# Kernel optimization log

Hardware: AMD Instinct MI355X
Metric: run time of the kernel (lower is better)

The kernel has to match this reference:

```python
import jax, jax.numpy as jnp
import numpy as np

BETA = 0.25
NUM_EMBEDDINGS = 2048
EMBEDDING_DIM = 512
N_TOKENS = 32768


def setup_inputs() -> dict:
    key = jax.random.key(0)
    k_z, k_e = jax.random.split(key)
    z = jax.random.normal(k_z, (N_TOKENS, EMBEDDING_DIM), dtype=jnp.float32)
    # nn.Embedding weight init: uniform(-1/K, 1/K)
    lim = 1.0 / NUM_EMBEDDINGS
    embedding = jax.random.uniform(
        k_e, (NUM_EMBEDDINGS, EMBEDDING_DIM), dtype=jnp.float32,
        minval=-lim, maxval=lim)
    return {"z": z, "embedding": embedding}


def reference(z, embedding):
    # z: [N, D], embedding: [K, D]
    z = z.reshape(-1, EMBEDDING_DIM)
    # squared euclidean distance: ||z||^2 + ||e||^2 - 2 z e^T  -> [N, K]
    d = (jnp.sum(z * z, axis=1, keepdims=True)
         + jnp.sum(embedding * embedding, axis=1)
         - 2.0 * jnp.matmul(z, embedding.T))
    min_encoding_indices = jnp.argmin(d, axis=1)[:, None]          # [N, 1]
    z_q = embedding[min_encoding_indices[:, 0]]                    # [N, D] gather

    sg = jax.lax.stop_gradient
    loss = jnp.mean((sg(z_q) - z) ** 2) + BETA * jnp.mean((z_q - sg(z)) ** 2)

    # straight-through estimator
    z_q_st = z + sg(z_q - z)

    # avg_probs = mean of one-hot encodings == normalized code-usage histogram
    n = z.shape[0]
    counts = jnp.zeros((NUM_EMBEDDINGS,), dtype=z.dtype).at[
        min_encoding_indices[:, 0]].add(1.0)
    avg_probs = counts / n
    perplexity = jnp.exp(-jnp.sum(avg_probs * jnp.log(avg_probs + 1e-10)))

    return (z_q_st, min_encoding_indices, loss, perplexity)
```

## Files before the change

kernel.cpp:

```cpp
#include <hip/hip_runtime.h>
#include <hip/hip_bf16.h>

#define N_TOK 32768
#define DIM   512
#define NE    2048

#define IDX_OFF  (N_TOK * DIM)
#define LOSS_OFF (IDX_OFF + N_TOK)
#define PERP_OFF (LOSS_OFF + 1)

#define KB(x) ((size_t)(x) << 10)
#define EPS 4e-4f

typedef __attribute__((ext_vector_type(8))) short bf16x8;
typedef __attribute__((ext_vector_type(4))) float f32x4;

__device__ inline unsigned short f2bf(float f) {
  unsigned int x = __float_as_uint(f);
  x = x + 0x7fffu + ((x >> 16) & 1u);
  return (unsigned short)(x >> 16);
}
__device__ inline float bfround(float f) {
  return __uint_as_float((unsigned int)f2bf(f) << 16);
}

__global__ __launch_bounds__(256) void npsum_cvt_all(
    const float* __restrict__ z, const float* __restrict__ e,
    float* __restrict__ zsum, float* __restrict__ esum,
    unsigned short* __restrict__ zbf, unsigned short* __restrict__ ebf,
    int* __restrict__ counts) {
#pragma clang fp contract(off)
  const int bz = blockIdx.x;
  if (bz < 8) counts[bz * 256 + threadIdx.x] = 0;
  const bool isz = bz < (N_TOK / 16);
  const int blk = isz ? bz : bz - (N_TOK / 16);
  const float* x = isz ? z : e;
  float* outs = isz ? zsum : esum;
  unsigned short* xbf = isz ? zbf : ebf;

  int wave = threadIdx.x >> 6;
  int lane = threadIdx.x & 63;
  int grp = lane >> 4, l = lane & 15;
  int row = blk * 16 + wave * 4 + grp;
  {
    const float* a = x + (size_t)row * DIM;
    float L[4];
    #pragma unroll
    for (int b = 0; b < 4; ++b) {
      const float* p = a + b * 128 + l;
      float q[8];
      #pragma unroll
      for (int j = 0; j < 8; ++j) {
        float t = p[16 * j];
        float s = t * t;
        asm volatile("" : "+v"(s));
        q[j] = s;
      }
      float v = ((q[0] + q[1]) + (q[2] + q[3])) + ((q[4] + q[5]) + (q[6] + q[7]));
      v += __shfl_xor(v, 8);
      v += __shfl_xor(v, 4);
      v += __shfl_xor(v, 2);
      v += __shfl_xor(v, 1);
      L[b] = v;
    }
    if (l == 0) outs[row] = (L[0] + L[1]) + (L[2] + L[3]);
  }
  const float* blkp = x + (size_t)blk * 16 * DIM;
  unsigned short* ob = xbf + (size_t)blk * 16 * DIM;
  #pragma unroll
  for (int u = 0; u < 4; ++u) {
    size_t off = (size_t)(u * 256 + threadIdx.x) * 8;
    float4 a2 = *(const float4*)(blkp + off);
    float4 b2 = *(const float4*)(blkp + off + 4);
    unsigned short h[8] = {f2bf(a2.x), f2bf(a2.y), f2bf(a2.z), f2bf(a2.w),
                           f2bf(b2.x), f2bf(b2.y), f2bf(b2.z), f2bf(b2.w)};
    *(uint4*)(ob + off) = *(uint4*)h;
  }
}

__device__ inline void stage_half(const unsigned short* __restrict__ gsrc,
                                  unsigned short* lds, int w, int l) {
  const int swz_col = ((l & 7) ^ (l >> 3)) * 8;
  const int rsub = l >> 3;
  #pragma unroll
  for (int s4 = 0; s4 < 2; ++s4) {
    int s = w * 2 + s4;
    const unsigned short* g = gsrc + (size_t)(s * 8 + rsub) * DIM + swz_col;
    __builtin_amdgcn_global_load_lds(
        (const __attribute__((address_space(1))) unsigned int*)g,
        (__attribute__((address_space(3))) unsigned int*)(lds + s * 512),
        16, 0, 0);
  }
}

#define BAR()   asm volatile("s_barrier" ::: "memory")
#define VMCNT4  asm volatile("s_waitcnt vmcnt(4)" ::: "memory")
#define VMCNT0  asm volatile("s_waitcnt vmcnt(0)" ::: "memory")

__global__ __launch_bounds__(512, 2) void gemm_groupmin(
    const unsigned short* __restrict__ ebf, const unsigned short* __restrict__ zbf,
    const float* __restrict__ esum, float* __restrict__ groupmin,
    unsigned short* __restrict__ gmask) {
  extern __shared__ unsigned short smem[];
  unsigned short* As = smem;
  unsigned short* Bs = smem + 32768;

  const int tid = threadIdx.x;
  const int tb = blockIdx.x;
  const int cb = blockIdx.y;
  const int w = tid >> 6, l = tid & 63;
  const int lr = l & 15, lk = l >> 4;
  const int wrow = (w >> 2) * 128;
  const int wcol = (w & 3) * 64;

  f32x4 acc[8][4];
  #pragma unroll
  for (int i = 0; i < 8; ++i)
    #pragma unroll
    for (int j = 0; j < 4; ++j) acc[i][j] = (f32x4)(0.f);

  bf16x8 aR[8], bA[4], bB[4];

  const unsigned short* Ag = ebf + (size_t)(cb * 256) * DIM;
  const unsigned short* Bg = zbf + (size_t)(tb * 256) * DIM;

#define LOADA(slot, qm) do { \
  _Pragma("unroll") for (int i2 = 0; i2 < 4; ++i2) { \
    int R = wrow + (qm)*64 + i2*16 + lr; \
    int rbase = ((slot)*2 + (R>>7))*8192 + (R&127)*64; \
    aR[i2*2+0] = *(const bf16x8*)&As[rbase + (((lk    ) ^ (R&7))*8)]; \
    aR[i2*2+1] = *(const bf16x8*)&As[rbase + (((4 + lk) ^ (R&7))*8)]; \
  } } while (0)

#define LOADB(dst, slot, qn) do { \
  _Pragma("unroll") for (int j = 0; j < 2; ++j) { \
    int C = wcol + (qn)*32 + j*16 + lr; \
    int cbase = ((slot)*2 + (C>>7))*8192 + (C&127)*64; \
    dst[j*2+0] = *(const bf16x8*)&Bs[cbase + (((lk    ) ^ (C&7))*8)]; \
    dst[j*2+1] = *(const bf16x8*)&Bs[cbase + (((4 + lk) ^ (C&7))*8)]; \
  } } while (0)

#define MFMA16(qm, qn, bX) do { \
  __builtin_amdgcn_s_setprio(1); \
  _Pragma("unroll") for (int i2 = 0; i2 < 4; ++i2) \
    _Pragma("unroll") for (int j = 0; j < 2; ++j) { \
      acc[(qm)*4+i2][(qn)*2+j] = __builtin_amdgcn_mfma_f32_16x16x32_bf16( \
          aR[i2*2+0], bX[j*2+0], acc[(qm)*4+i2][(qn)*2+j], 0, 0, 0); \
      acc[(qm)*4+i2][(qn)*2+j] = __builtin_amdgcn_mfma_f32_16x16x32_bf16( \
          aR[i2*2+1], bX[j*2+1], acc[(qm)*4+i2][(qn)*2+j], 0, 0, 0); \
    } \
  __builtin_amdgcn_s_setprio(0); \
} while (0)

  stage_half(Bg,                 Bs,             w, l);
  stage_half(Bg + 128 * DIM,     Bs + 8192,      w, l);
  stage_half(Ag,                 As,             w, l);
  stage_half(Ag + 128 * DIM,     As + 8192,      w, l);
  stage_half(Bg + 64,            Bs + 2 * 8192,  w, l);
  stage_half(Bg + 128 * DIM + 64, Bs + 3 * 8192, w, l);
  VMCNT4;
  BAR();

  #pragma unroll
  for (int i = 0; i < 4; ++i) {
    const int t1k = (2 * i + 1) * 64;
    const int u0k = (2 * i + 2) * 64;
    const int u1k = (2 * i + 3) * 64;
    LOADA(0, 0); LOADB(bA, 0, 0); LOADB(bB, 0, 1);
    stage_half(Ag + t1k, As + 2 * 8192, w, l);
    BAR(); MFMA16(0, 0, bA);
    stage_half(Ag + 128 * DIM + t1k, As + 3 * 8192, w, l);
    BAR(); MFMA16(0, 1, bB);
    LOADA(0, 1);
    if (i < 3) stage_half(Bg + u0k, Bs, w, l);
    BAR(); MFMA16(1, 0, bA);
    if (i < 3) stage_half(Bg + 128 * DIM + u0k, Bs + 8192, w, l);
    BAR(); MFMA16(1, 1, bB);
    if (i < 3) { VMCNT4; } else { VMCNT0; }
    BAR();
    LOADA(1, 0); LOADB(bA, 1, 0); LOADB(bB, 1, 1);
    if (i < 3) stage_half(Ag + u0k, As, w, l);
    BAR(); MFMA16(0, 0, bA);
    if (i < 3) stage_half(Ag + 128 * DIM + u0k, As + 8192, w, l);
    BAR(); MFMA16(0, 1, bB);
    LOADA(1, 1);
    if (i < 3) stage_half(Bg + u1k, Bs + 2 * 8192, w, l);
    BAR(); MFMA16(1, 0, bA);
    if (i < 3) stage_half(Bg + 128 * DIM + u1k, Bs + 3 * 8192, w, l);
    BAR(); MFMA16(1, 1, bB);
    if (i < 3) { VMCNT4; BAR(); }
  }

  float esr[8][4];
  #pragma unroll
  for (int i = 0; i < 8; ++i)
    #pragma unroll
    for (int q = 0; q < 4; ++q)
      esr[i][q] = esum[cb * 256 + wrow + i * 16 + lk * 4 + q];

  float m8[4][8];
  unsigned short k8[4][8];
  #pragma unroll
  for (int i = 0; i < 8; ++i) {
    #pragma unroll
    for (int j = 0; j < 4; ++j) {
      float v0 = fmaf(-2.f, acc[i][j][0], esr[i][0]);
      float v1 = fmaf(-2.f, acc[i][j][1], esr[i][1]);
      float v2 = fmaf(-2.f, acc[i][j][2], esr[i][2]);
      float v3 = fmaf(-2.f, acc[i][j][3], esr[i][3]);
      float m = fminf(fminf(v0, v1), fminf(v2, v3));
      m = fminf(m, __shfl_xor(m, 16));
      m = fminf(m, __shfl_xor(m, 32));
      float gl = m + EPS;
      int mk = (((v0 <= gl) ? 1 : 0) | ((v1 <= gl) ? 2 : 0) |
                ((v2 <= gl) ? 4 : 0) | ((v3 <= gl) ? 8 : 0)) << (lk * 4);
      mk |= __shfl_xor(mk, 16);
      mk |= __shfl_xor(mk, 32);
      m8[j][i] = m;
      k8[j][i] = (unsigned short)mk;
    }
  }
  if (lk == 0) {
    #pragma unroll
    for (int j = 0; j < 4; ++j) {
      int token = tb * 256 + wcol + j * 16 + lr;
      size_t gb = (size_t)token * 128 + cb * 16 + (w >> 2) * 8;
      float4 f0 = {m8[j][0], m8[j][1], m8[j][2], m8[j][3]};
      float4 f1 = {m8[j][4], m8[j][5], m8[j][6], m8[j][7]};
      *(float4*)&groupmin[gb] = f0;
      *(float4*)&groupmin[gb + 4] = f1;
      *(uint4*)&gmask[gb] = *(uint4*)&k8[j][0];
    }
  }
#undef LOADA
#undef LOADB
#undef MFMA16
}

__global__ __launch_bounds__(256) void select_exact(
    const float* __restrict__ z, const float* __restrict__ e,
    const float* __restrict__ zsum, const float* __restrict__ esum,
    const float* __restrict__ groupmin, const unsigned short* __restrict__ gmask,
    int* __restrict__ idx_final, int* __restrict__ counts,
    float* __restrict__ out, float* __restrict__ lossp) {
  __shared__ float lred[4];
  const int wid = threadIdx.x >> 6;
  const int t = blockIdx.x * 4 + wid;
  const int lane = threadIdx.x & 63;
  const float* zr = z + (size_t)t * DIM;

  float4 za = *(const float4*)(zr + lane * 4);
  float4 zb = *(const float4*)(zr + 256 + lane * 4);

  float g0 = groupmin[(size_t)t * 128 + lane];
  float g1 = groupmin[(size_t)t * 128 + 64 + lane];
  int msk0 = gmask[(size_t)t * 128 + lane];
  int msk1 = gmask[(size_t)t * 128 + 64 + lane];
  float m = fminf(g0, g1);
  #pragma unroll
  for (int s = 32; s >= 1; s >>= 1) m = fminf(m, __shfl_xor(m, s));
  float lim = m + EPS;
  unsigned long long mm0 = __ballot(g0 <= lim);
  unsigned long long mm1 = __ballot(g1 <= lim);
  float zst = zsum[t];
  float bd = 3.402823466e38f; int bc = 0x7fffffff;

  #pragma unroll 1
  for (int half = 0; half < 2; ++half) {
    unsigned long long mk = half ? mm1 : mm0;
    while (mk) {
      int b = __ffsll((unsigned long long)mk) - 1;
      mk &= mk - 1;
      const int base = (half * 64 + b) * 16;
      unsigned gm = (unsigned)__shfl(half ? msk1 : msk0, b) & 0xFFFFu;
      while (gm) {
        int ci = __ffs(gm) - 1;
        gm &= gm - 1;
        int c = base + ci;
        const float* er = e + (size_t)c * DIM;
        float4 ea = *(const float4*)(er + lane * 4);
        float4 eb = *(const float4*)(er + 256 + lane * 4);
        float p = 0.f;
        p = fmaf(za.x, ea.x, p); p = fmaf(za.y, ea.y, p);
        p = fmaf(za.z, ea.z, p); p = fmaf(za.w, ea.w, p);
        p = fmaf(zb.x, eb.x, p); p = fmaf(zb.y, eb.y, p);
        p = fmaf(zb.z, eb.z, p); p = fmaf(zb.w, eb.w, p);
        #pragma unroll
        for (int s = 1; s <= 32; s <<= 1) p += __shfl_xor(p, s);
        float d = (zst + esum[c]) - 2.f * p;
        if (d < bd) { bd = d; bc = c; }
      }
    }
  }
  if (lane == 0) {
    idx_final[t] = bc;
    out[IDX_OFF + t] = bfround((float)bc);
    atomicAdd(&counts[bc], 1);
    lred[wid] = bd;
  }
  __syncthreads();
  if (threadIdx.x == 0)
    lossp[blockIdx.x] = (lred[0] + lred[1]) + (lred[2] + lred[3]);
}

__global__ __launch_bounds__(256) void scatter_fin(
    const float* __restrict__ e, const int* __restrict__ idx_final,
    const int* __restrict__ counts, const float* __restrict__ lossp,
    float* __restrict__ out) {
  if (blockIdx.x == N_TOK / 8) {
    __shared__ float red[4], red2[4];
    int tid = threadIdx.x;
    float s = 0.f;
    for (int j = tid; j < NE; j += 256) {
      float p = (float)counts[j] * (1.0f / (float)N_TOK);
      s += p * logf(p + 1e-10f);
    }
    float ls = 0.f;
    for (int j = tid; j < N_TOK / 4; j += 256) ls += lossp[j];
    #pragma unroll
    for (int m = 32; m >= 1; m >>= 1) {
      s += __shfl_xor(s, m);
      ls += __shfl_xor(ls, m);
    }
    if ((tid & 63) == 0) { red[tid >> 6] = s; red2[tid >> 6] = ls; }
    __syncthreads();
    if (tid == 0) {
      float tot = red[0] + red[1] + red[2] + red[3];
      float lt = red2[0] + red2[1] + red2[2] + red2[3];
      out[PERP_OFF] = bfround(expf(-tot));
      out[LOSS_OFF] = bfround(lt * 1.25f / (float)(N_TOK * DIM));
    }
    return;
  }
  int t = blockIdx.x * 8 + (threadIdx.x >> 5);
  int g = threadIdx.x & 31;
  int idx = idx_final[t] & (NE - 1);
  const float* er = e + (size_t)idx * DIM;
  float* op = out + (size_t)t * DIM;
  #pragma unroll
  for (int p = 0; p < 4; ++p) {
    int c = p * 128 + g * 4;
    float4 ev = *(const float4*)(er + c);
    float4 ov;
    ov.x = bfround(ev.x); ov.y = bfround(ev.y);
    ov.z = bfround(ev.z); ov.w = bfround(ev.w);
    *(float4*)(op + c) = ov;
  }
}

extern "C" void kernel_launch(void* const* d_in, const int* in_sizes, int n_in,
                              void* d_out, int out_size, void* d_ws, size_t ws_size,
                              hipStream_t stream) {
  const float* z = (const float*)d_in[0];
  const float* e = (const float*)d_in[1];
  float* out = (float*)d_out;
  char* ws = (char*)d_ws;

  float*    zsum      = (float*)(ws + KB(0));
  float*    esum      = (float*)(ws + KB(128));
  int*      counts    = (int*)(ws + KB(136));
  float*    lossp     = (float*)(ws + KB(144));
  int*      idx_final = (int*)(ws + KB(176));
  unsigned short* ebf = (unsigned short*)(ws + KB(304));

  unsigned short* zbf = (unsigned short*)out;
  float* groupmin = out + 8388608;
  unsigned short* gmask = (unsigned short*)(out + 12582912);

  npsum_cvt_all<<<N_TOK / 16 + NE / 16, 256, 0, stream>>>(
      z, e, zsum, esum, zbf, ebf, counts);
  gemm_groupmin<<<dim3(N_TOK / 256, NE / 256), 512, 131072, stream>>>(
      ebf, zbf, esum, groupmin, gmask);
  select_exact<<<N_TOK / 4, 256, 0, stream>>>(z, e, zsum, esum, groupmin, gmask,
                                              idx_final, counts, out, lossp);
  scatter_fin<<<N_TOK / 8 + 1, 256, 0, stream>>>(e, idx_final, counts, lossp, out);
}
```

Baseline: 157.8 us.

## Pack group min and mask into one word and fuse gather into select

The GEMM epilogue now writes one 32-bit word per group, holding a bf16-rounded group minimum and a 16-bit candidate mask, instead of separate float and ushort arrays. This cuts intermediate write and read traffic. Because the bf16 minimum is coarser, the selection threshold is widened, which can add extra candidates to the exact rescoring. When the workspace is large enough, the packed buffer lives there instead of in the output, so select_exact can also gather and write z_q directly. That removes the separate scatter kernel's re-read of indices and embeddings and leaves only a single-block finalize launch.

```diff
diff --git a/kernel.cpp b/kernel.cpp
--- a/kernel.cpp
+++ b/kernel.cpp
@@ -11,6 +11,7 @@
 
 #define KB(x) ((size_t)(x) << 10)
 #define EPS 4e-4f
+#define EPS_SEL 1e-3f
 
 typedef __attribute__((ext_vector_type(8))) short bf16x8;
 typedef __attribute__((ext_vector_type(4))) float f32x4;
@@ -99,8 +100,7 @@
 
 __global__ __launch_bounds__(512, 2) void gemm_groupmin(
     const unsigned short* __restrict__ ebf, const unsigned short* __restrict__ zbf,
-    const float* __restrict__ esum, float* __restrict__ groupmin,
-    unsigned short* __restrict__ gmask) {
+    const float* __restrict__ esum, unsigned* __restrict__ gmv) {
   extern __shared__ unsigned short smem[];
   unsigned short* As = smem;
   unsigned short* Bs = smem + 32768;
@@ -198,8 +198,7 @@
     for (int q = 0; q < 4; ++q)
       esr[i][q] = esum[cb * 256 + wrow + i * 16 + lk * 4 + q];
 
-  float m8[4][8];
-  unsigned short k8[4][8];
+  unsigned gmv8[4][8];
   #pragma unroll
   for (int i = 0; i < 8; ++i) {
     #pragma unroll
@@ -216,8 +215,7 @@
                 ((v2 <= gl) ? 4 : 0) | ((v3 <= gl) ? 8 : 0)) << (lk * 4);
       mk |= __shfl_xor(mk, 16);
       mk |= __shfl_xor(mk, 32);
-      m8[j][i] = m;
-      k8[j][i] = (unsigned short)mk;
+      gmv8[j][i] = ((unsigned)f2bf(m) << 16) | (unsigned)(mk & 0xFFFF);
     }
   }
   if (lk == 0) {
@@ -225,11 +223,10 @@
     for (int j = 0; j < 4; ++j) {
       int token = tb * 256 + wcol + j * 16 + lr;
       size_t gb = (size_t)token * 128 + cb * 16 + (w >> 2) * 8;
-      float4 f0 = {m8[j][0], m8[j][1], m8[j][2], m8[j][3]};
-      float4 f1 = {m8[j][4], m8[j][5], m8[j][6], m8[j][7]};
-      *(float4*)&groupmin[gb] = f0;
-      *(float4*)&groupmin[gb + 4] = f1;
-      *(uint4*)&gmask[gb] = *(uint4*)&k8[j][0];
+      uint4 q0 = {gmv8[j][0], gmv8[j][1], gmv8[j][2], gmv8[j][3]};
+      uint4 q1 = {gmv8[j][4], gmv8[j][5], gmv8[j][6], gmv8[j][7]};
+      *(uint4*)&gmv[gb] = q0;
+      *(uint4*)&gmv[gb + 4] = q1;
     }
   }
 #undef LOADA
@@ -240,9 +237,9 @@
 __global__ __launch_bounds__(256) void select_exact(
     const float* __restrict__ z, const float* __restrict__ e,
     const float* __restrict__ zsum, const float* __restrict__ esum,
-    const float* __restrict__ groupmin, const unsigned short* __restrict__ gmask,
+    const unsigned* __restrict__ gmv,
     int* __restrict__ idx_final, int* __restrict__ counts,
-    float* __restrict__ out, float* __restrict__ lossp) {
+    float* __restrict__ out, float* __restrict__ lossp, int fused) {
   __shared__ float lred[4];
   const int wid = threadIdx.x >> 6;
   const int t = blockIdx.x * 4 + wid;
@@ -252,14 +249,14 @@
   float4 za = *(const float4*)(zr + lane * 4);
   float4 zb = *(const float4*)(zr + 256 + lane * 4);
 
-  float g0 = groupmin[(size_t)t * 128 + lane];
-  float g1 = groupmin[(size_t)t * 128 + 64 + lane];
-  int msk0 = gmask[(size_t)t * 128 + lane];
-  int msk1 = gmask[(size_t)t * 128 + 64 + lane];
+  unsigned u0 = gmv[(size_t)t * 128 + lane];
+  unsigned u1 = gmv[(size_t)t * 128 + 64 + lane];
+  float g0 = __uint_as_float(u0 & 0xFFFF0000u);
+  float g1 = __uint_as_float(u1 & 0xFFFF0000u);
   float m = fminf(g0, g1);
   #pragma unroll
   for (int s = 32; s >= 1; s >>= 1) m = fminf(m, __shfl_xor(m, s));
-  float lim = m + EPS;
+  float lim = m + EPS_SEL;
   unsigned long long mm0 = __ballot(g0 <= lim);
   unsigned long long mm1 = __ballot(g1 <= lim);
   float zst = zsum[t];
@@ -272,7 +269,7 @@
       int b = __ffsll((unsigned long long)mk) - 1;
       mk &= mk - 1;
       const int base = (half * 64 + b) * 16;
-      unsigned gm = (unsigned)__shfl(half ? msk1 : msk0, b) & 0xFFFFu;
+      unsigned gm = (unsigned)__shfl((int)(half ? u1 : u0), b) & 0xFFFFu;
       while (gm) {
         int ci = __ffs(gm) - 1;
         gm &= gm - 1;
@@ -292,6 +289,19 @@
       }
     }
   }
+  if (fused) {
+    const float* er = e + (size_t)(bc & (NE - 1)) * DIM;
+    float4 ea = *(const float4*)(er + lane * 4);
+    float4 eb = *(const float4*)(er + 256 + lane * 4);
+    float* op = out + (size_t)t * DIM;
+    float4 oa, ob;
+    oa.x = bfround(ea.x); oa.y = bfround(ea.y);
+    oa.z = bfround(ea.z); oa.w = bfround(ea.w);
+    ob.x = bfround(eb.x); ob.y = bfround(eb.y);
+    ob.z = bfround(eb.z); ob.w = bfround(eb.w);
+    *(float4*)(op + lane * 4) = oa;
+    *(float4*)(op + 256 + lane * 4) = ob;
+  }
   if (lane == 0) {
     idx_final[t] = bc;
     out[IDX_OFF + t] = bfround((float)bc);
@@ -303,35 +313,44 @@
     lossp[blockIdx.x] = (lred[0] + lred[1]) + (lred[2] + lred[3]);
 }
 
+__device__ inline void finalize_body(const int* __restrict__ counts,
+                                     const float* __restrict__ lossp,
+                                     float* __restrict__ out) {
+  __shared__ float red[4], red2[4];
+  int tid = threadIdx.x;
+  float s = 0.f;
+  for (int j = tid; j < NE; j += 256) {
+    float p = (float)counts[j] * (1.0f / (float)N_TOK);
+    s += p * logf(p + 1e-10f);
+  }
+  float ls = 0.f;
+  for (int j = tid; j < N_TOK / 4; j += 256) ls += lossp[j];
+  #pragma unroll
+  for (int m = 32; m >= 1; m >>= 1) {
+    s += __shfl_xor(s, m);
+    ls += __shfl_xor(ls, m);
+  }
+  if ((tid & 63) == 0) { red[tid >> 6] = s; red2[tid >> 6] = ls; }
+  __syncthreads();
+  if (tid == 0) {
+    float tot = red[0] + red[1] + red[2] + red[3];
+    float lt = red2[0] + red2[1] + red2[2] + red2[3];
+    out[PERP_OFF] = bfround(expf(-tot));
+    out[LOSS_OFF] = bfround(lt * 1.25f / (float)(N_TOK * DIM));
+  }
+}
+
+__global__ __launch_bounds__(256) void fin_only(
+    const int* __restrict__ counts, const float* __restrict__ lossp,
+    float* __restrict__ out) {
+  finalize_body(counts, lossp, out);
+}
+
 __global__ __launch_bounds__(256) void scatter_fin(
     const float* __restrict__ e, const int* __restrict__ idx_final,
     const int* __restrict__ counts, const float* __restrict__ lossp,
     float* __restrict__ out) {
-  if (blockIdx.x == N_TOK / 8) {
-    __shared__ float red[4], red2[4];
-    int tid = threadIdx.x;
-    float s = 0.f;
-    for (int j = tid; j < NE; j += 256) {
-      float p = (float)counts[j] * (1.0f / (float)N_TOK);
-      s += p * logf(p + 1e-10f);
-    }
-    float ls = 0.f;
-    for (int j = tid; j < N_TOK / 4; j += 256) ls += lossp[j];
-    #pragma unroll
-    for (int m = 32; m >= 1; m >>= 1) {
-      s += __shfl_xor(s, m);
-      ls += __shfl_xor(ls, m);
-    }
-    if ((tid & 63) == 0) { red[tid >> 6] = s; red2[tid >> 6] = ls; }
-    __syncthreads();
-    if (tid == 0) {
-      float tot = red[0] + red[1] + red[2] + red[3];
-      float lt = red2[0] + red2[1] + red2[2] + red2[3];
-      out[PERP_OFF] = bfround(expf(-tot));
-      out[LOSS_OFF] = bfround(lt * 1.25f / (float)(N_TOK * DIM));
-    }
-    return;
-  }
+  if (blockIdx.x == N_TOK / 8) { finalize_body(counts, lossp, out); return; }
   int t = blockIdx.x * 8 + (threadIdx.x >> 5);
   int g = threadIdx.x & 31;
   int idx = idx_final[t] & (NE - 1);
@@ -364,14 +383,23 @@
   unsigned short* ebf = (unsigned short*)(ws + KB(304));
 
   unsigned short* zbf = (unsigned short*)out;
-  float* groupmin = out + 8388608;
-  unsigned short* gmask = (unsigned short*)(out + 12582912);
+
+  const size_t gmv_off = KB(2368);
+  const size_t gmv_bytes = (size_t)N_TOK * 128 * 4;
+  const bool fused = ws_size >= gmv_off + gmv_bytes;
+  unsigned* gmv = fused ? (unsigned*)(ws + gmv_off)
+                        : (unsigned*)(out + 8388608);
 
   npsum_cvt_all<<<N_TOK / 16 + NE / 16, 256, 0, stream>>>(
       z, e, zsum, esum, zbf, ebf, counts);
   gemm_groupmin<<<dim3(N_TOK / 256, NE / 256), 512, 131072, stream>>>(
-      ebf, zbf, esum, groupmin, gmask);
-  select_exact<<<N_TOK / 4, 256, 0, stream>>>(z, e, zsum, esum, groupmin, gmask,
-                                              idx_final, counts, out, lossp);
-  scatter_fin<<<N_TOK / 8 + 1, 256, 0, stream>>>(e, idx_final, counts, lossp, out);
-}
+      ebf, zbf, esum, gmv);
+  select_exact<<<N_TOK / 4, 256, 0, stream>>>(z, e, zsum, esum, gmv,
+                                              idx_final, counts, out, lossp,
+                                              fused ? 1 : 0);
+  if (fused) {
+    fin_only<<<1, 256, 0, stream>>>(counts, lossp, out);
+  } else {
+    scatter_fin<<<N_TOK / 8 + 1, 256, 0, stream>>>(e, idx_final, counts, lossp, out);
+  }
+}
```

After: 156.6 us. About the same (-0.8%).
